# Performance work log

Measured on AMD Instinct MI355X. Metric: run time of the kernel, lower is better.

Reference implementation:

```python
import jax, jax.numpy as jnp
import numpy as np

WS = 7   # window_size
SS = 3   # shift_size = window_size // 2
NH = 16  # num_heads


def _rel_pos_index(ws):
    coords = np.stack(np.meshgrid(np.arange(ws), np.arange(ws), indexing='ij'))  # (2, ws, ws)
    cf = coords.reshape(2, -1)
    rel = (cf[:, :, None] - cf[:, None, :]).transpose(1, 2, 0)
    rel[:, :, 0] += ws - 1
    rel[:, :, 1] += ws - 1
    rel[:, :, 0] *= 2 * ws - 1
    return rel.sum(-1)  # (ws*ws, ws*ws) int

REL_IDX = _rel_pos_index(WS)


def _attn_mask(h, w, ws, ss):
    img = np.zeros((h, w))
    sls = (slice(0, -ws), slice(-ws, -ss), slice(-ss, None))
    cnt = 0
    for i in sls:
        for j in sls:
            img[i, j] = cnt
            cnt += 1
    mw = img.reshape(h // ws, ws, w // ws, ws).transpose(0, 2, 1, 3).reshape(-1, ws * ws)
    d = mw[:, None, :] - mw[:, :, None]  # (nW, N, N)
    return np.where(d != 0, -100.0, 0.0).astype(np.float32)


def _part(x, ws):
    b, h, w, c = x.shape
    return x.reshape(b, h // ws, ws, w // ws, ws, c).transpose(0, 1, 3, 2, 4, 5).reshape(-1, ws * ws, c)


def _rev(win, ws, h, w):
    c = win.shape[-1]
    b = win.shape[0] // ((h // ws) * (w // ws))
    return win.reshape(b, h // ws, w // ws, ws, ws, c).transpose(0, 1, 3, 2, 4, 5).reshape(b, h, w, c)


def _ln(x, g, b):
    m = x.mean(-1, keepdims=True)
    v = x.var(-1, keepdims=True)
    return (x - m) / jnp.sqrt(v + 1e-5) * g + b


def _wattn(x, qkv_w, qkv_b, proj_w, proj_b, table, mask):
    B_, N, C = x.shape
    hd = C // NH
    scale = hd ** -0.5
    qkv = (x @ qkv_w.T + qkv_b).reshape(B_, N, 3, NH, hd).transpose(2, 0, 3, 1, 4)
    q, k, v = qkv[0] * scale, qkv[1], qkv[2]  # (B_, NH, N, hd)
    attn = jnp.einsum('bhnd,bhmd->bhnm', q, k)
    bias = table[REL_IDX.reshape(-1)].reshape(N, N, NH).transpose(2, 0, 1)  # (NH, N, N)
    attn = attn + bias[None]
    if mask is not None:
        nW = mask.shape[0]
        attn = (attn.reshape(B_ // nW, nW, NH, N, N) + mask[None, :, None]).reshape(B_, NH, N, N)
    attn = jax.nn.softmax(attn, axis=-1)
    out = jnp.einsum('bhnm,bhmd->bhnd', attn, v).transpose(0, 2, 1, 3).reshape(B_, N, C)
    return out @ proj_w.T + proj_b


def _mlp(x, w1, b1, w2, b2):
    return jax.nn.gelu(x @ w1.T + b1, approximate=False) @ w2.T + b2


def _forward(x, w_norm1_g, w_norm1_b, w_qkv_w, w_qkv_b, w_proj_w, w_proj_b, w_table,
             w_norm2_g, w_norm2_b, w_fc1_w, w_fc1_b, w_fc2_w, w_fc2_b,
             sw_norm1_g, sw_norm1_b, sw_qkv_w, sw_qkv_b, sw_proj_w, sw_proj_b, sw_table,
             sw_norm2_g, sw_norm2_b, sw_fc1_w, sw_fc1_b, sw_fc2_w, sw_fc2_b):
    b, c, h, w = x.shape
    x = jnp.transpose(x, (0, 2, 3, 1)).reshape(b, h * w, c)  # (B, HW, C)
    shortcut = x
    xn = _ln(x, w_norm1_g, w_norm1_b).reshape(b, h, w, c)
    aw = _wattn(_part(xn, WS), w_qkv_w, w_qkv_b, w_proj_w, w_proj_b, w_table, None)
    x = shortcut + _rev(aw, WS, h, w).reshape(b, h * w, c)
    x = x + _mlp(_ln(x, w_norm2_g, w_norm2_b), w_fc1_w, w_fc1_b, w_fc2_w, w_fc2_b)
    # shifted-window branch (shift_size > 0 since min(h,w) > window_size)
    xn = _ln(x, sw_norm1_g, sw_norm1_b)
    mask = jnp.asarray(_attn_mask(h, w, WS, SS))
    shifted = jnp.roll(xn.reshape(b, h, w, c), (-SS, -SS), axis=(1, 2))
    sa = _wattn(_part(shifted, WS), sw_qkv_w, sw_qkv_b, sw_proj_w, sw_proj_b, sw_table, mask)
    shifted = jnp.roll(_rev(sa, WS, h, w), (SS, SS), axis=(1, 2)).reshape(b, h * w, c)
    # NOTE: source adds the residual to the *normalized* activations here; kept faithful.
    x = xn + shifted
    x = x + _mlp(_ln(x, sw_norm2_g, sw_norm2_b), sw_fc1_w, sw_fc1_b, sw_fc2_w, sw_fc2_b)
    return x.reshape(b, h, w, c)


def setup_inputs() -> dict:
    key = jax.random.key(0)
    ks = jax.random.split(key, 32)
    B, C, H, W = 8, 512, 56, 56
    Cm = 4 * C
    T = (2 * WS - 1) ** 2

    def rn(k, shape, s=0.02):
        return jax.random.normal(k, shape, jnp.float32) * s

    d = {'x': jax.random.normal(ks[0], (B, C, H, W), jnp.float32)}
    for i, p in enumerate(['w', 'sw']):
        o = 1 + i * 6
        d[p + '_norm1_g'] = jnp.ones((C,), jnp.float32)
        d[p + '_norm1_b'] = jnp.zeros((C,), jnp.float32)
        d[p + '_qkv_w'] = rn(ks[o], (3 * C, C))
        d[p + '_qkv_b'] = jnp.zeros((3 * C,), jnp.float32)
        d[p + '_proj_w'] = rn(ks[o + 1], (C, C))
        d[p + '_proj_b'] = jnp.zeros((C,), jnp.float32)
        d[p + '_table'] = rn(ks[o + 2], (T, NH))
        d[p + '_norm2_g'] = jnp.ones((C,), jnp.float32)
        d[p + '_norm2_b'] = jnp.zeros((C,), jnp.float32)
        d[p + '_fc1_w'] = rn(ks[o + 3], (Cm, C))
        d[p + '_fc1_b'] = jnp.zeros((Cm,), jnp.float32)
        d[p + '_fc2_w'] = rn(ks[o + 4], (C, Cm))
        d[p + '_fc2_b'] = jnp.zeros((C,), jnp.float32)
    return d


def reference(x, w_norm1_g, w_norm1_b, w_qkv_w, w_qkv_b, w_proj_w, w_proj_b, w_table,
              w_norm2_g, w_norm2_b, w_fc1_w, w_fc1_b, w_fc2_w, w_fc2_b,
              sw_norm1_g, sw_norm1_b, sw_qkv_w, sw_qkv_b, sw_proj_w, sw_proj_b, sw_table,
              sw_norm2_g, sw_norm2_b, sw_fc1_w, sw_fc1_b, sw_fc2_w, sw_fc2_b):
    return _forward(x, w_norm1_g, w_norm1_b, w_qkv_w, w_qkv_b, w_proj_w, w_proj_b, w_table,
                    w_norm2_g, w_norm2_b, w_fc1_w, w_fc1_b, w_fc2_w, w_fc2_b,
                    sw_norm1_g, sw_norm1_b, sw_qkv_w, sw_qkv_b, sw_proj_w, sw_proj_b, sw_table,
                    sw_norm2_g, sw_norm2_b, sw_fc1_w, sw_fc1_b, sw_fc2_w, sw_fc2_b)
```

## Files before the change

### kernel.cpp

```cpp
#include <hip/hip_runtime.h>
#include <hip/hip_bf16.h>

using bf16 = __hip_bfloat16;

#define B_      8
#define C_      512
#define H_      56
#define W_      56
#define HW_     3136
#define M_      25088
#define NH_     16
#define HD_     32
#define WS_     7
#define NT_     49

typedef __attribute__((ext_vector_type(8))) short bf16x8;
typedef __attribute__((ext_vector_type(4))) float f32x4;

#define AS1(p) ((const __attribute__((address_space(1))) void*)(p))
#define AS3(p) ((__attribute__((address_space(3))) void*)(p))

__device__ inline float bf2f(const bf16 v) {
    unsigned short u = *reinterpret_cast<const unsigned short*>(&v);
    return __uint_as_float((unsigned)u << 16);
}
__device__ inline unsigned short f2bfu(float f) {
    bf16 h = __float2bfloat16(f);
    return *reinterpret_cast<unsigned short*>(&h);
}
__device__ inline float rdv(const float* p) { return *p; }
__device__ inline float rdv(const bf16* p)  { return bf2f(*p); }
__device__ inline void stv(float* p, float v) { *p = v; }
__device__ inline void stv(bf16* p, float v)  { *p = __float2bfloat16(v); }

__device__ inline float gelu_t(float v) {
    const float u = v * (0.79788456080286536f + 0.035677408136300125f * v * v);
    const float e = __expf(2.0f * u);
    return 0.5f * v * (2.0f - 2.0f / (e + 1.0f));
}

__global__ void k_detect(const void* g1, int* flag) {
    const unsigned short* u = (const unsigned short*)g1;
    *flag = (u[0] == 0x3F80u) ? 1 : 0;
}

struct WArgs {
    const void* src[26];
    bf16*       dst[26];
    int         n[26];
};
__global__ __launch_bounds__(256) void k_convert_all(WArgs a, const int* flag) {
    const int isb = *flag;
    const int gid = blockIdx.x * 256 + threadIdx.x;
    const int stride = gridDim.x * 256;
    #pragma unroll 1
    for (int w = 0; w < 26; ++w) {
        const int n = a.n[w];
        bf16* d = a.dst[w];
        if (isb) {
            const unsigned short* s = (const unsigned short*)a.src[w];
            for (int i = gid; i < n; i += stride) ((unsigned short*)d)[i] = s[i];
        } else {
            const float* s = (const float*)a.src[w];
            for (int i = gid; i < n; i += stride) d[i] = __float2bfloat16(s[i]);
        }
    }
}

__global__ __launch_bounds__(256) void k_transpose_in(const void* xin, bf16* X,
                                                      const int* flag) {
    __shared__ float tile[32][33];
    const int isb = *flag;
    const int p0 = blockIdx.x * 32, c0 = blockIdx.y * 32, b = blockIdx.z;
    const int tp = threadIdx.x & 31, tc = threadIdx.x >> 5;
    const size_t ibase = (size_t)b * C_ * HW_;
    #pragma unroll
    for (int i = 0; i < 4; ++i) {
        const int c = tc + i * 8;
        const size_t idx = ibase + (size_t)(c0 + c) * HW_ + p0 + tp;
        tile[c][tp] = isb ? bf2f(((const bf16*)xin)[idx]) : ((const float*)xin)[idx];
    }
    __syncthreads();
    const int wc = threadIdx.x & 31, wp = threadIdx.x >> 5;
    bf16* dst = X + (size_t)b * HW_ * C_;
    #pragma unroll
    for (int i = 0; i < 4; ++i) {
        const int p = wp + i * 8;
        dst[(size_t)(p0 + p) * C_ + c0 + wc] = __float2bfloat16(tile[wc][p]);
    }
}

__global__ __launch_bounds__(128) void k_layernorm(const bf16* __restrict__ X,
                                                   const bf16* __restrict__ g,
                                                   const bf16* __restrict__ bta,
                                                   bf16* __restrict__ XN) {
    const int tok = blockIdx.x;
    const ushort4 u = reinterpret_cast<const ushort4*>(X + (size_t)tok * C_)[threadIdx.x];
    float4 v;
    v.x = __uint_as_float((unsigned)u.x << 16);
    v.y = __uint_as_float((unsigned)u.y << 16);
    v.z = __uint_as_float((unsigned)u.z << 16);
    v.w = __uint_as_float((unsigned)u.w << 16);
    float s  = v.x + v.y + v.z + v.w;
    float s2 = v.x * v.x + v.y * v.y + v.z * v.z + v.w * v.w;
    #pragma unroll
    for (int o = 32; o > 0; o >>= 1) { s += __shfl_down(s, o); s2 += __shfl_down(s2, o); }
    __shared__ float sh[4];
    if ((threadIdx.x & 63) == 0) { sh[threadIdx.x >> 6] = s; sh[2 + (threadIdx.x >> 6)] = s2; }
    __syncthreads();
    const float ts = sh[0] + sh[1], ts2 = sh[2] + sh[3];
    const float m = ts * (1.0f / C_);
    const float var = ts2 * (1.0f / C_) - m * m;
    const float r = rsqrtf(var + 1e-5f);
    const int c = threadIdx.x * 4;
    ushort4 o;
    o.x = f2bfu((v.x - m) * r * bf2f(g[c + 0]) + bf2f(bta[c + 0]));
    o.y = f2bfu((v.y - m) * r * bf2f(g[c + 1]) + bf2f(bta[c + 1]));
    o.z = f2bfu((v.z - m) * r * bf2f(g[c + 2]) + bf2f(bta[c + 2]));
    o.w = f2bfu((v.w - m) * r * bf2f(g[c + 3]) + bf2f(bta[c + 3]));
    reinterpret_cast<ushort4*>(XN + (size_t)tok * C_)[threadIdx.x] = o;
}

template <typename TADD, typename TO, bool GELU, bool ADD, bool FINAL>
__global__ __launch_bounds__(512, 2) void k_gemm_mfma(const bf16* __restrict__ A,
                                                      const bf16* __restrict__ Wt,
                                                      const bf16* __restrict__ bias,
                                                      const TADD* __restrict__ addp,
                                                      TO* __restrict__ out,
                                                      const int* flag,
                                                      int N, int K) {
    __shared__ bf16 sA[2][256 * 64];
    __shared__ bf16 sB[2][256 * 64];
    const int tid  = threadIdx.x;
    const int lane = tid & 63;
    const int wid  = tid >> 6;
    const int wr   = wid >> 2;
    const int wc2  = wid & 3;

    const int nwg  = gridDim.x;
    const int orig = blockIdx.x;
    const int nx = nwg >> 3, rr_ = nwg & 7;
    const int xcd = orig & 7, offw = orig >> 3;
    const int wg = (xcd < rr_ ? xcd * (nx + 1) : rr_ * (nx + 1) + (xcd - rr_) * nx) + offw;
    const int gx = N >> 8;
    const int m0 = (wg / gx) * 256, n0 = (wg % gx) * 256;

    const f32x4 vz = {0.f, 0.f, 0.f, 0.f};
    f32x4 acc[8][4];
    #pragma unroll
    for (int i = 0; i < 8; ++i)
        #pragma unroll
        for (int j = 0; j < 4; ++j) acc[i][j] = vz;

    const int sr8  = lane >> 3;
    const int schk = (lane & 7) ^ sr8;
    const bf16* gA0 = A  + (size_t)(m0 + sr8) * K + schk * 8;
    const bf16* gB0 = Wt + (size_t)(n0 + sr8) * K + schk * 8;

    const int l15 = lane & 15, g4 = lane >> 4;
    const int NTLE = K >> 6;

    int cur = 0;
    {
        #pragma unroll
        for (int p = 0; p < 4; ++p) {
            const int q = wid * 4 + p;
            __builtin_amdgcn_global_load_lds(AS1(gA0 + (size_t)(q * 8) * K),
                                             AS3(&sA[0][q * 512]), 16, 0, 0);
            __builtin_amdgcn_global_load_lds(AS1(gB0 + (size_t)(q * 8) * K),
                                             AS3(&sB[0][q * 512]), 16, 0, 0);
        }
    }

    for (int t = 0; t < NTLE; ++t) {
        asm volatile("s_waitcnt vmcnt(0)" ::: "memory");
        __builtin_amdgcn_s_barrier();

        if (t + 1 < NTLE) {
            const int kt = (t + 1) << 6;
            #pragma unroll
            for (int p = 0; p < 4; ++p) {
                const int q = wid * 4 + p;
                __builtin_amdgcn_global_load_lds(AS1(gA0 + (size_t)(q * 8) * K + kt),
                                                 AS3(&sA[cur ^ 1][q * 512]), 16, 0, 0);
                __builtin_amdgcn_global_load_lds(AS1(gB0 + (size_t)(q * 8) * K + kt),
                                                 AS3(&sB[cur ^ 1][q * 512]), 16, 0, 0);
            }
        }

        bf16x8 bfr[4][2];
        #pragma unroll
        for (int ks = 0; ks < 2; ++ks) {
            const int ch = ((ks << 2) | g4) ^ (l15 & 7);
            #pragma unroll
            for (int j = 0; j < 4; ++j) {
                const int rowB = wc2 * 64 + j * 16 + l15;
                bfr[j][ks] = *reinterpret_cast<const bf16x8*>(&sB[cur][rowB * 64 + ch * 8]);
            }
        }
        const int ch0 = g4 ^ (l15 & 7);
        const int ch1 = (4 | g4) ^ (l15 & 7);
        __builtin_amdgcn_s_setprio(1);
        #pragma unroll
        for (int i = 0; i < 8; ++i) {
            const int rowA = wr * 128 + i * 16 + l15;
            const bf16x8 a0 = *reinterpret_cast<const bf16x8*>(&sA[cur][rowA * 64 + ch0 * 8]);
            const bf16x8 a1 = *reinterpret_cast<const bf16x8*>(&sA[cur][rowA * 64 + ch1 * 8]);
            #pragma unroll
            for (int j = 0; j < 4; ++j) {
                acc[i][j] = __builtin_amdgcn_mfma_f32_16x16x32_bf16(a0, bfr[j][0], acc[i][j], 0, 0, 0);
                acc[i][j] = __builtin_amdgcn_mfma_f32_16x16x32_bf16(a1, bfr[j][1], acc[i][j], 0, 0, 0);
            }
        }
        __builtin_amdgcn_s_setprio(0);

        asm volatile("s_waitcnt lgkmcnt(0)" ::: "memory");
        __builtin_amdgcn_s_barrier();
        cur ^= 1;
    }

    int obf = 0;
    if constexpr (FINAL) obf = *flag;
    const int colBase = n0 + wc2 * 64 + l15;
    const int rowTop  = m0 + wr * 128 + g4 * 4;
    #pragma unroll
    for (int j = 0; j < 4; ++j) {
        const int col = colBase + j * 16;
        const float bc = bf2f(bias[col]);
        #pragma unroll
        for (int i = 0; i < 8; ++i) {
            #pragma unroll
            for (int r = 0; r < 4; ++r) {
                const int row = rowTop + i * 16 + r;
                float v = acc[i][j][r] + bc;
                if constexpr (GELU) v = gelu_t(v);
                if constexpr (ADD)  v += rdv(&addp[(size_t)row * N + col]);
                if constexpr (FINAL) {
                    if (obf) ((bf16*)(void*)out)[(size_t)row * N + col] = __float2bfloat16(v);
                    else     ((float*)(void*)out)[(size_t)row * N + col] = v;
                } else {
                    stv(&out[(size_t)row * N + col], v);
                }
            }
        }
    }
}

__global__ __launch_bounds__(256) void k_mktbl(const bf16* __restrict__ table,
                                               bf16* __restrict__ out, int shifted) {
    const int bh = blockIdx.x;
    const int cls = bh >> 4, h = bh & 15;
    const int rowE = shifted ? (cls >> 1) : 0;
    const int colE = shifted ? (cls & 1) : 0;
    for (int e = threadIdx.x; e < 64 * 64; e += 256) {
        const int i = e >> 6, j = e & 63;
        float v;
        if (i < NT_ && j < NT_) {
            const int yi = i / WS_, xi = i % WS_, yj = j / WS_, xj = j % WS_;
            const int ridx = (yi - yj + 6) * 13 + (xi - xj + 6);
            v = bf2f(table[ridx * NH_ + h]);
            const int ri = (rowE ? (yi < 4 ? 1 : 2) : 0) * 3 + (colE ? (xi < 4 ? 1 : 2) : 0);
            const int rj = (rowE ? (yj < 4 ? 1 : 2) : 0) * 3 + (colE ? (xj < 4 ? 1 : 2) : 0);
            if (ri != rj) v -= 100.f;
        } else if (j >= NT_) {
            v = -3e30f;
        } else {
            v = 0.f;
        }
        out[((size_t)bh << 12) + e] = __float2bfloat16(v);
    }
}

template <int SS, bool SHIFTED>
__global__ __launch_bounds__(64) void k_attn_mfma(const bf16* __restrict__ QKV,
                                                  const bf16* __restrict__ tbl,
                                                  bf16* __restrict__ O) {
    __shared__ __align__(16) short uQK[5120];
    __shared__ __align__(16) short uVt[2304];
    __shared__ int toks[NT_];
    short* Qs = uQK;
    short* Ks = uQK + 2560;
    short* Ps = uQK;

    const int lane = threadIdx.x;
    const int head = blockIdx.x & 15;
    const int win  = blockIdx.x >> 4;
    const int bl = win >> 6, w64 = win & 63;
    const int wy = w64 >> 3, wx = w64 & 7;

    if (lane < NT_) {
        const int dy = lane / WS_, dx = lane % WS_;
        const int sr = wy * WS_ + dy, scn = wx * WS_ + dx;
        const int r = (sr + SS) % H_, c = (scn + SS) % W_;
        toks[lane] = bl * HW_ + r * W_ + c;
    }
    __syncthreads();

    const int g4 = lane >> 4, l15 = lane & 15;
    const int tsg = lane >> 2, csg = (lane & 3) * 8;

    #pragma unroll
    for (int rr = 0; rr < 4; ++rr) {
        const int t = rr * 16 + tsg;
        bf16x8 qv = {0,0,0,0,0,0,0,0}, kv = {0,0,0,0,0,0,0,0}, vv = {0,0,0,0,0,0,0,0};
        if (t < NT_) {
            const bf16* base = QKV + (size_t)toks[t] * 1536 + head * HD_ + csg;
            qv = *reinterpret_cast<const bf16x8*>(base);
            kv = *reinterpret_cast<const bf16x8*>(base + 512);
            vv = *reinterpret_cast<const bf16x8*>(base + 1024);
        }
        *reinterpret_cast<bf16x8*>(&Qs[t * 40 + csg]) = qv;
        *reinterpret_cast<bf16x8*>(&Ks[t * 40 + csg]) = kv;
        #pragma unroll
        for (int e = 0; e < 8; ++e) uVt[(csg + e) * 72 + t] = ((const short*)&vv)[e];
    }
    __syncthreads();

    bf16x8 aq[4], bk[4];
    #pragma unroll
    for (int f = 0; f < 4; ++f) {
        aq[f] = *reinterpret_cast<const bf16x8*>(&Qs[(f * 16 + l15) * 40 + g4 * 8]);
        bk[f] = *reinterpret_cast<const bf16x8*>(&Ks[(f * 16 + l15) * 40 + g4 * 8]);
    }
    const f32x4 vz = {0.f, 0.f, 0.f, 0.f};
    f32x4 sacc[4][4];
    #pragma unroll
    for (int qi = 0; qi < 4; ++qi)
        #pragma unroll
        for (int kj = 0; kj < 4; ++kj)
            sacc[qi][kj] = __builtin_amdgcn_mfma_f32_16x16x32_bf16(aq[qi], bk[kj], vz, 0, 0, 0);
    __syncthreads();

    const int cls = SHIFTED ? (((wy == 7) ? 2 : 0) + ((wx == 7) ? 1 : 0)) : 0;
    const bf16* tb = tbl + (((size_t)(cls * NH_ + head)) << 12);
    const float scale = 0.17677669529663687f;
    #pragma unroll
    for (int qi = 0; qi < 4; ++qi) {
        #pragma unroll
        for (int r = 0; r < 4; ++r) {
            const int i = qi * 16 + g4 * 4 + r;
            const bf16* trow = tb + (i << 6);
            float sv[4];
            #pragma unroll
            for (int kj = 0; kj < 4; ++kj)
                sv[kj] = sacc[qi][kj][r] * scale + bf2f(trow[kj * 16 + l15]);
            float mx = fmaxf(fmaxf(sv[0], sv[1]), fmaxf(sv[2], sv[3]));
            #pragma unroll
            for (int d = 1; d <= 8; d <<= 1) mx = fmaxf(mx, __shfl_xor(mx, d));
            float p[4], sum = 0.f;
            #pragma unroll
            for (int kj = 0; kj < 4; ++kj) { p[kj] = __expf(sv[kj] - mx); sum += p[kj]; }
            #pragma unroll
            for (int d = 1; d <= 8; d <<= 1) sum += __shfl_xor(sum, d);
            const float inv = 1.0f / sum;
            #pragma unroll
            for (int kj = 0; kj < 4; ++kj)
                Ps[i * 72 + kj * 16 + l15] = (short)f2bfu(p[kj] * inv);
        }
    }
    __syncthreads();

    f32x4 oacc[4][2];
    #pragma unroll
    for (int qi = 0; qi < 4; ++qi) { oacc[qi][0] = vz; oacc[qi][1] = vz; }
    #pragma unroll
    for (int ks = 0; ks < 2; ++ks) {
        bf16x8 bv[2];
        #pragma unroll
        for (int dj = 0; dj < 2; ++dj)
            bv[dj] = *reinterpret_cast<const bf16x8*>(&uVt[(dj * 16 + l15) * 72 + ks * 32 + g4 * 8]);
        #pragma unroll
        for (int qi = 0; qi < 4; ++qi) {
            const bf16x8 ap = *reinterpret_cast<const bf16x8*>(&Ps[(qi * 16 + l15) * 72 + ks * 32 + g4 * 8]);
            #pragma unroll
            for (int dj = 0; dj < 2; ++dj)
                oacc[qi][dj] = __builtin_amdgcn_mfma_f32_16x16x32_bf16(ap, bv[dj], oacc[qi][dj], 0, 0, 0);
        }
    }
    #pragma unroll
    for (int qi = 0; qi < 4; ++qi) {
        #pragma unroll
        for (int r = 0; r < 4; ++r) {
            const int i = qi * 16 + g4 * 4 + r;
            if (i < NT_) {
                const size_t ob = (size_t)toks[i] * C_ + head * HD_ + l15;
                O[ob]      = __float2bfloat16(oacc[qi][0][r]);
                O[ob + 16] = __float2bfloat16(oacc[qi][1][r]);
            }
        }
    }
}

extern "C" void kernel_launch(void* const* d_in, const int* in_sizes, int n_in,
                              void* d_out, int out_size, void* d_ws, size_t ws_size,
                              hipStream_t stream) {
    (void)out_size; (void)ws_size;
    char* ws = (char*)d_ws;
    const size_t WEIGHT_RESERVE = 12651520;
    bf16*  WC   = (bf16*)ws;
    int*   FLG  = (int*)(ws + WEIGHT_RESERVE);
    bf16*  TBL1 = (bf16*)(ws + WEIGHT_RESERVE + 1024);
    bf16*  TBL2 = (bf16*)(ws + WEIGHT_RESERVE + 1024 + 131072);
    bf16*  X    = (bf16*)(ws + WEIGHT_RESERVE + 656384);
    bf16*  XN   = X + (size_t)M_ * C_;
    char*  BIG  = (char*)(XN + (size_t)M_ * C_);

    size_t offs[27];
    size_t off = 0;
    for (int i = 1; i < n_in && i < 27; ++i) { offs[i] = off; off += (size_t)((in_sizes[i] + 7) & ~7); }
    auto wc = [&](int i) { return (const bf16*)(WC + offs[i]); };

    k_detect<<<1, 1, 0, stream>>>(d_in[1], FLG);
    {
        WArgs a;
        for (int i = 1; i < 27; ++i) {
            a.src[i - 1] = d_in[i];
            a.dst[i - 1] = WC + offs[i];
            a.n[i - 1]   = in_sizes[i];
        }
        k_convert_all<<<512, 256, 0, stream>>>(a, FLG);
    }
    k_mktbl<<<16, 256, 0, stream>>>(wc(7),  TBL1, 0);
    k_mktbl<<<64, 256, 0, stream>>>(wc(20), TBL2, 1);

    const dim3 gT(HW_ / 32, C_ / 32, B_);
    k_transpose_in<<<gT, 256, 0, stream>>>(d_in[0], X, FLG);

    bf16* QKV = (bf16*)BIG;
    bf16* ATT = (bf16*)(BIG + (size_t)M_ * 1536 * 2);
    bf16* HID = (bf16*)BIG;

    const int gQ = (1536 / 256) * (M_ / 256);
    const int gP = (512 / 256)  * (M_ / 256);
    const int gF = (2048 / 256) * (M_ / 256);
    const dim3 gA(B_ * 64 * NH_);

    k_layernorm<<<M_, 128, 0, stream>>>(X, wc(1), wc(2), XN);
    k_gemm_mfma<bf16, bf16, false, false, false><<<gQ, 512, 0, stream>>>(
        XN, wc(3), wc(4), (const bf16*)nullptr, QKV, nullptr, 1536, C_);
    k_attn_mfma<0, false><<<gA, 64, 0, stream>>>(QKV, TBL1, ATT);
    k_gemm_mfma<bf16, bf16, false, true, false><<<gP, 512, 0, stream>>>(
        ATT, wc(5), wc(6), X, X, nullptr, C_, C_);
    k_layernorm<<<M_, 128, 0, stream>>>(X, wc(8), wc(9), XN);
    k_gemm_mfma<bf16, bf16, true, false, false><<<gF, 512, 0, stream>>>(
        XN, wc(10), wc(11), (const bf16*)nullptr, HID, nullptr, 2048, C_);
    k_gemm_mfma<bf16, bf16, false, true, false><<<gP, 512, 0, stream>>>(
        HID, wc(12), wc(13), X, X, nullptr, C_, 2048);
    k_layernorm<<<M_, 128, 0, stream>>>(X, wc(14), wc(15), XN);
    k_gemm_mfma<bf16, bf16, false, false, false><<<gQ, 512, 0, stream>>>(
        XN, wc(16), wc(17), (const bf16*)nullptr, QKV, nullptr, 1536, C_);
    k_attn_mfma<3, true><<<gA, 64, 0, stream>>>(QKV, TBL2, ATT);
    k_gemm_mfma<bf16, bf16, false, true, false><<<gP, 512, 0, stream>>>(
        ATT, wc(18), wc(19), XN, X, nullptr, C_, C_);
    k_layernorm<<<M_, 128, 0, stream>>>(X, wc(21), wc(22), XN);
    k_gemm_mfma<bf16, bf16, true, false, false><<<gF, 512, 0, stream>>>(
        XN, wc(23), wc(24), (const bf16*)nullptr, HID, nullptr, 2048, C_);
    k_gemm_mfma<bf16, float, false, true, true><<<gP, 512, 0, stream>>>(
        HID, wc(25), wc(26), X, (float*)d_out, FLG, C_, 2048);
}
```

Before: 910.5 us.

## Split GEMM into shallow-K high-occupancy and 128x128 tile variants

Replaces the single 256x256x64 GEMM kernel with two variants. The first keeps 256x256 output tiles but uses a 32-deep K slice, halving LDS use so four workgroups can fit per CU. The second uses 128x128 tiles with 256 threads for the N=512 projection and fc2 GEMMs, giving more workgroups to fill the GPU where the 256-wide tiling produced few blocks. It also reorders the epilogue so the bias values are loaded once up front. The cost is more barrier iterations per K in the first variant and less operand reuse per tile in the second.

```diff
diff --git a/kernel.cpp b/kernel.cpp
--- a/kernel.cpp
+++ b/kernel.cpp
@@ -122,15 +122,15 @@
 }
 
 template <typename TADD, typename TO, bool GELU, bool ADD, bool FINAL>
-__global__ __launch_bounds__(512, 2) void k_gemm_mfma(const bf16* __restrict__ A,
-                                                      const bf16* __restrict__ Wt,
-                                                      const bf16* __restrict__ bias,
-                                                      const TADD* __restrict__ addp,
-                                                      TO* __restrict__ out,
-                                                      const int* flag,
-                                                      int N, int K) {
-    __shared__ bf16 sA[2][256 * 64];
-    __shared__ bf16 sB[2][256 * 64];
+__global__ __launch_bounds__(512, 4) void k_gemm_mfma_a(const bf16* __restrict__ A,
+                                                        const bf16* __restrict__ Wt,
+                                                        const bf16* __restrict__ bias,
+                                                        const TADD* __restrict__ addp,
+                                                        TO* __restrict__ out,
+                                                        const int* flag,
+                                                        int N, int K) {
+    __shared__ bf16 sA[2][256 * 32];
+    __shared__ bf16 sB[2][256 * 32];
     const int tid  = threadIdx.x;
     const int lane = tid & 63;
     const int wid  = tid >> 6;
@@ -152,6 +152,125 @@
         #pragma unroll
         for (int j = 0; j < 4; ++j) acc[i][j] = vz;
 
+    const int sr16 = lane >> 2;
+    const int schk = (lane & 3) ^ ((lane >> 3) & 3);
+    const bf16* gA0 = A  + (size_t)(m0 + sr16) * K + schk * 8;
+    const bf16* gB0 = Wt + (size_t)(n0 + sr16) * K + schk * 8;
+
+    const int l15 = lane & 15, g4 = lane >> 4;
+    const int NT32 = K >> 5;
+
+    int cur = 0;
+    {
+        #pragma unroll
+        for (int p = 0; p < 2; ++p) {
+            const int q = wid * 2 + p;
+            __builtin_amdgcn_global_load_lds(AS1(gA0 + (size_t)(q * 16) * K),
+                                             AS3(&sA[0][q * 512]), 16, 0, 0);
+            __builtin_amdgcn_global_load_lds(AS1(gB0 + (size_t)(q * 16) * K),
+                                             AS3(&sB[0][q * 512]), 16, 0, 0);
+        }
+    }
+
+    for (int t = 0; t < NT32; ++t) {
+        asm volatile("s_waitcnt vmcnt(0)" ::: "memory");
+        __builtin_amdgcn_s_barrier();
+
+        if (t + 1 < NT32) {
+            const int kt = (t + 1) << 5;
+            #pragma unroll
+            for (int p = 0; p < 2; ++p) {
+                const int q = wid * 2 + p;
+                __builtin_amdgcn_global_load_lds(AS1(gA0 + (size_t)(q * 16) * K + kt),
+                                                 AS3(&sA[cur ^ 1][q * 512]), 16, 0, 0);
+                __builtin_amdgcn_global_load_lds(AS1(gB0 + (size_t)(q * 16) * K + kt),
+                                                 AS3(&sB[cur ^ 1][q * 512]), 16, 0, 0);
+            }
+        }
+
+        const int ch = g4 ^ ((l15 >> 1) & 3);
+        bf16x8 bfr[4];
+        #pragma unroll
+        for (int j = 0; j < 4; ++j) {
+            const int rowB = wc2 * 64 + j * 16 + l15;
+            bfr[j] = *reinterpret_cast<const bf16x8*>(&sB[cur][rowB * 32 + ch * 8]);
+        }
+        __builtin_amdgcn_s_setprio(1);
+        #pragma unroll
+        for (int i = 0; i < 8; ++i) {
+            const int rowA = wr * 128 + i * 16 + l15;
+            const bf16x8 a0 = *reinterpret_cast<const bf16x8*>(&sA[cur][rowA * 32 + ch * 8]);
+            #pragma unroll
+            for (int j = 0; j < 4; ++j)
+                acc[i][j] = __builtin_amdgcn_mfma_f32_16x16x32_bf16(a0, bfr[j], acc[i][j], 0, 0, 0);
+        }
+        __builtin_amdgcn_s_setprio(0);
+
+        asm volatile("s_waitcnt lgkmcnt(0)" ::: "memory");
+        __builtin_amdgcn_s_barrier();
+        cur ^= 1;
+    }
+
+    int obf = 0;
+    if constexpr (FINAL) obf = *flag;
+    const int colBase = n0 + wc2 * 64 + l15;
+    const int rowTop  = m0 + wr * 128 + g4 * 4;
+    float bc[4];
+    #pragma unroll
+    for (int j = 0; j < 4; ++j) bc[j] = bf2f(bias[colBase + j * 16]);
+    #pragma unroll
+    for (int i = 0; i < 8; ++i) {
+        #pragma unroll
+        for (int r = 0; r < 4; ++r) {
+            const int row = rowTop + i * 16 + r;
+            #pragma unroll
+            for (int j = 0; j < 4; ++j) {
+                const int col = colBase + j * 16;
+                float v = acc[i][j][r] + bc[j];
+                if constexpr (GELU) v = gelu_t(v);
+                if constexpr (ADD)  v += rdv(&addp[(size_t)row * N + col]);
+                if constexpr (FINAL) {
+                    if (obf) ((bf16*)(void*)out)[(size_t)row * N + col] = __float2bfloat16(v);
+                    else     ((float*)(void*)out)[(size_t)row * N + col] = v;
+                } else {
+                    stv(&out[(size_t)row * N + col], v);
+                }
+            }
+        }
+    }
+}
+
+template <typename TADD, typename TO, bool GELU, bool ADD, bool FINAL>
+__global__ __launch_bounds__(256, 2) void k_gemm_mfma_b(const bf16* __restrict__ A,
+                                                        const bf16* __restrict__ Wt,
+                                                        const bf16* __restrict__ bias,
+                                                        const TADD* __restrict__ addp,
+                                                        TO* __restrict__ out,
+                                                        const int* flag,
+                                                        int N, int K) {
+    __shared__ bf16 sA[2][128 * 64];
+    __shared__ bf16 sB[2][128 * 64];
+    const int tid  = threadIdx.x;
+    const int lane = tid & 63;
+    const int wid  = tid >> 6;
+    const int wr   = wid >> 1;
+    const int wc2  = wid & 1;
+
+    const int nwg  = gridDim.x;
+    const int orig = blockIdx.x;
+    const int nx = nwg >> 3, rr_ = nwg & 7;
+    const int xcd = orig & 7, offw = orig >> 3;
+    const int wg = (xcd < rr_ ? xcd * (nx + 1) : rr_ * (nx + 1) + (xcd - rr_) * nx) + offw;
+    const int gx = N >> 7;
+    const int m0 = (wg / gx) * 128, n0 = (wg % gx) * 128;
+
+    const f32x4 vz = {0.f, 0.f, 0.f, 0.f};
+    f32x4 acc[4][4];
+    #pragma unroll
+    for (int i = 0; i < 4; ++i)
+        #pragma unroll
+        for (int j = 0; j < 4; ++j) acc[i][j] = vz;
+
     const int sr8  = lane >> 3;
     const int schk = (lane & 7) ^ sr8;
     const bf16* gA0 = A  + (size_t)(m0 + sr8) * K + schk * 8;
@@ -188,30 +307,27 @@
             }
         }
 
-        bf16x8 bfr[4][2];
+        bf16x8 af[4][2], bf_[4][2];
         #pragma unroll
         for (int ks = 0; ks < 2; ++ks) {
             const int ch = ((ks << 2) | g4) ^ (l15 & 7);
             #pragma unroll
+            for (int f = 0; f < 4; ++f) {
+                const int rowA = wr * 64 + f * 16 + l15;
+                af[f][ks] = *reinterpret_cast<const bf16x8*>(&sA[cur][rowA * 64 + ch * 8]);
+                const int rowB = wc2 * 64 + f * 16 + l15;
+                bf_[f][ks] = *reinterpret_cast<const bf16x8*>(&sB[cur][rowB * 64 + ch * 8]);
+            }
+        }
+
+        __builtin_amdgcn_s_setprio(1);
+        #pragma unroll
+        for (int i = 0; i < 4; ++i)
+            #pragma unroll
             for (int j = 0; j < 4; ++j) {
-                const int rowB = wc2 * 64 + j * 16 + l15;
-                bfr[j][ks] = *reinterpret_cast<const bf16x8*>(&sB[cur][rowB * 64 + ch * 8]);
-            }
-        }
-        const int ch0 = g4 ^ (l15 & 7);
-        const int ch1 = (4 | g4) ^ (l15 & 7);
-        __builtin_amdgcn_s_setprio(1);
-        #pragma unroll
-        for (int i = 0; i < 8; ++i) {
-            const int rowA = wr * 128 + i * 16 + l15;
-            const bf16x8 a0 = *reinterpret_cast<const bf16x8*>(&sA[cur][rowA * 64 + ch0 * 8]);
-            const bf16x8 a1 = *reinterpret_cast<const bf16x8*>(&sA[cur][rowA * 64 + ch1 * 8]);
-            #pragma unroll
-            for (int j = 0; j < 4; ++j) {
-                acc[i][j] = __builtin_amdgcn_mfma_f32_16x16x32_bf16(a0, bfr[j][0], acc[i][j], 0, 0, 0);
-                acc[i][j] = __builtin_amdgcn_mfma_f32_16x16x32_bf16(a1, bfr[j][1], acc[i][j], 0, 0, 0);
-            }
-        }
+                acc[i][j] = __builtin_amdgcn_mfma_f32_16x16x32_bf16(af[i][0], bf_[j][0], acc[i][j], 0, 0, 0);
+                acc[i][j] = __builtin_amdgcn_mfma_f32_16x16x32_bf16(af[i][1], bf_[j][1], acc[i][j], 0, 0, 0);
+            }
         __builtin_amdgcn_s_setprio(0);
 
         asm volatile("s_waitcnt lgkmcnt(0)" ::: "memory");
@@ -222,17 +338,19 @@
     int obf = 0;
     if constexpr (FINAL) obf = *flag;
     const int colBase = n0 + wc2 * 64 + l15;
-    const int rowTop  = m0 + wr * 128 + g4 * 4;
-    #pragma unroll
-    for (int j = 0; j < 4; ++j) {
-        const int col = colBase + j * 16;
-        const float bc = bf2f(bias[col]);
-        #pragma unroll
-        for (int i = 0; i < 8; ++i) {
-            #pragma unroll
-            for (int r = 0; r < 4; ++r) {
-                const int row = rowTop + i * 16 + r;
-                float v = acc[i][j][r] + bc;
+    const int rowTop  = m0 + wr * 64 + g4 * 4;
+    float bc[4];
+    #pragma unroll
+    for (int j = 0; j < 4; ++j) bc[j] = bf2f(bias[colBase + j * 16]);
+    #pragma unroll
+    for (int i = 0; i < 4; ++i) {
+        #pragma unroll
+        for (int r = 0; r < 4; ++r) {
+            const int row = rowTop + i * 16 + r;
+            #pragma unroll
+            for (int j = 0; j < 4; ++j) {
+                const int col = colBase + j * 16;
+                float v = acc[i][j][r] + bc[j];
                 if constexpr (GELU) v = gelu_t(v);
                 if constexpr (ADD)  v += rdv(&addp[(size_t)row * N + col]);
                 if constexpr (FINAL) {
@@ -431,30 +549,30 @@
     bf16* HID = (bf16*)BIG;
 
     const int gQ = (1536 / 256) * (M_ / 256);
-    const int gP = (512 / 256)  * (M_ / 256);
     const int gF = (2048 / 256) * (M_ / 256);
+    const int gP = (512 / 128)  * (M_ / 128);
     const dim3 gA(B_ * 64 * NH_);
 
     k_layernorm<<<M_, 128, 0, stream>>>(X, wc(1), wc(2), XN);
-    k_gemm_mfma<bf16, bf16, false, false, false><<<gQ, 512, 0, stream>>>(
+    k_gemm_mfma_a<bf16, bf16, false, false, false><<<gQ, 512, 0, stream>>>(
         XN, wc(3), wc(4), (const bf16*)nullptr, QKV, nullptr, 1536, C_);
     k_attn_mfma<0, false><<<gA, 64, 0, stream>>>(QKV, TBL1, ATT);
-    k_gemm_mfma<bf16, bf16, false, true, false><<<gP, 512, 0, stream>>>(
+    k_gemm_mfma_b<bf16, bf16, false, true, false><<<gP, 256, 0, stream>>>(
         ATT, wc(5), wc(6), X, X, nullptr, C_, C_);
     k_layernorm<<<M_, 128, 0, stream>>>(X, wc(8), wc(9), XN);
-    k_gemm_mfma<bf16, bf16, true, false, false><<<gF, 512, 0, stream>>>(
+    k_gemm_mfma_a<bf16, bf16, true, false, false><<<gF, 512, 0, stream>>>(
         XN, wc(10), wc(11), (const bf16*)nullptr, HID, nullptr, 2048, C_);
-    k_gemm_mfma<bf16, bf16, false, true, false><<<gP, 512, 0, stream>>>(
+    k_gemm_mfma_b<bf16, bf16, false, true, false><<<gP, 256, 0, stream>>>(
         HID, wc(12), wc(13), X, X, nullptr, C_, 2048);
     k_layernorm<<<M_, 128, 0, stream>>>(X, wc(14), wc(15), XN);
-    k_gemm_mfma<bf16, bf16, false, false, false><<<gQ, 512, 0, stream>>>(
+    k_gemm_mfma_a<bf16, bf16, false, false, false><<<gQ, 512, 0, stream>>>(
         XN, wc(16), wc(17), (const bf16*)nullptr, QKV, nullptr, 1536, C_);
     k_attn_mfma<3, true><<<gA, 64, 0, stream>>>(QKV, TBL2, ATT);
-    k_gemm_mfma<bf16, bf16, false, true, false><<<gP, 512, 0, stream>>>(
+    k_gemm_mfma_b<bf16, bf16, false, true, false><<<gP, 256, 0, stream>>>(
         ATT, wc(18), wc(19), XN, X, nullptr, C_, C_);
     k_layernorm<<<M_, 128, 0, stream>>>(X, wc(21), wc(22), XN);
-    k_gemm_mfma<bf16, bf16, true, false, false><<<gF, 512, 0, stream>>>(
+    k_gemm_mfma_a<bf16, bf16, true, false, false><<<gF, 512, 0, stream>>>(
         XN, wc(23), wc(24), (const bf16*)nullptr, HID, nullptr, 2048, C_);
-    k_gemm_mfma<bf16, float, false, true, true><<<gP, 512, 0, stream>>>(
+    k_gemm_mfma_b<bf16, float, false, true, true><<<gP, 256, 0, stream>>>(
         HID, wc(25), wc(26), X, (float*)d_out, FLG, C_, 2048);
 }
```

Measured after the change: 1.912 ms. 2.1x slower.

## Use 256x128 GEMM tiles with triple-buffered LDS prefetch and partial vmcnt waits

Applied to the files above, without the earlier changes.

Shrinks the GEMM tile from 256x256 to 256x128, halving per-wave accumulators and doubling the grid. Replaces the double buffer with a three-stage LDS ring, issuing loads three tiles ahead and waiting with partial vmcnt counts so global loads overlap compute. Also reorders the epilogue loops and hoists the bias loads. LDS use per block rises to about 144KB, which may limit occupancy, and the smaller tile lowers arithmetic intensity.

```diff
diff --git a/kernel.cpp b/kernel.cpp
--- a/kernel.cpp
+++ b/kernel.cpp
@@ -129,26 +129,26 @@
                                                       TO* __restrict__ out,
                                                       const int* flag,
                                                       int N, int K) {
-    __shared__ bf16 sA[2][256 * 64];
-    __shared__ bf16 sB[2][256 * 64];
+    __shared__ bf16 sA[3][256 * 64];
+    __shared__ bf16 sB[3][128 * 64];
     const int tid  = threadIdx.x;
     const int lane = tid & 63;
     const int wid  = tid >> 6;
-    const int wr   = wid >> 2;
-    const int wc2  = wid & 3;
+    const int wr   = wid >> 1;
+    const int wc2  = wid & 1;
 
     const int nwg  = gridDim.x;
     const int orig = blockIdx.x;
     const int nx = nwg >> 3, rr_ = nwg & 7;
     const int xcd = orig & 7, offw = orig >> 3;
     const int wg = (xcd < rr_ ? xcd * (nx + 1) : rr_ * (nx + 1) + (xcd - rr_) * nx) + offw;
-    const int gx = N >> 8;
-    const int m0 = (wg / gx) * 256, n0 = (wg % gx) * 256;
+    const int gx = N >> 7;
+    const int m0 = (wg / gx) * 256, n0 = (wg % gx) * 128;
 
     const f32x4 vz = {0.f, 0.f, 0.f, 0.f};
-    f32x4 acc[8][4];
-    #pragma unroll
-    for (int i = 0; i < 8; ++i)
+    f32x4 acc[4][4];
+    #pragma unroll
+    for (int i = 0; i < 4; ++i)
         #pragma unroll
         for (int j = 0; j < 4; ++j) acc[i][j] = vz;
 
@@ -160,79 +160,94 @@
     const int l15 = lane & 15, g4 = lane >> 4;
     const int NTLE = K >> 6;
 
-    int cur = 0;
-    {
+    #pragma unroll
+    for (int tt = 0; tt < 3; ++tt) {
+        const int kt = tt << 6;
         #pragma unroll
         for (int p = 0; p < 4; ++p) {
             const int q = wid * 4 + p;
-            __builtin_amdgcn_global_load_lds(AS1(gA0 + (size_t)(q * 8) * K),
-                                             AS3(&sA[0][q * 512]), 16, 0, 0);
-            __builtin_amdgcn_global_load_lds(AS1(gB0 + (size_t)(q * 8) * K),
-                                             AS3(&sB[0][q * 512]), 16, 0, 0);
+            __builtin_amdgcn_global_load_lds(AS1(gA0 + (size_t)(q * 8) * K + kt),
+                                             AS3(&sA[tt][q * 512]), 16, 0, 0);
+        }
+        #pragma unroll
+        for (int p = 0; p < 2; ++p) {
+            const int q = wid * 2 + p;
+            __builtin_amdgcn_global_load_lds(AS1(gB0 + (size_t)(q * 8) * K + kt),
+                                             AS3(&sB[tt][q * 512]), 16, 0, 0);
         }
     }
 
     for (int t = 0; t < NTLE; ++t) {
-        asm volatile("s_waitcnt vmcnt(0)" ::: "memory");
+        const int rem = NTLE - 1 - t;
+        if (rem >= 2)      asm volatile("s_waitcnt vmcnt(12)" ::: "memory");
+        else if (rem == 1) asm volatile("s_waitcnt vmcnt(6)"  ::: "memory");
+        else               asm volatile("s_waitcnt vmcnt(0)"  ::: "memory");
         __builtin_amdgcn_s_barrier();
 
-        if (t + 1 < NTLE) {
-            const int kt = (t + 1) << 6;
+        const int buf = t % 3;
+        bf16x8 bfr[4][2];
+        #pragma unroll
+        for (int ks = 0; ks < 2; ++ks) {
+            const int ch = ((ks << 2) | g4) ^ (l15 & 7);
+            #pragma unroll
+            for (int j = 0; j < 4; ++j) {
+                const int rowB = wc2 * 64 + j * 16 + l15;
+                bfr[j][ks] = *reinterpret_cast<const bf16x8*>(&sB[buf][rowB * 64 + ch * 8]);
+            }
+        }
+        const int ch0 = g4 ^ (l15 & 7);
+        const int ch1 = (4 | g4) ^ (l15 & 7);
+        __builtin_amdgcn_s_setprio(1);
+        #pragma unroll
+        for (int i = 0; i < 4; ++i) {
+            const int rowA = wr * 64 + i * 16 + l15;
+            const bf16x8 a0 = *reinterpret_cast<const bf16x8*>(&sA[buf][rowA * 64 + ch0 * 8]);
+            const bf16x8 a1 = *reinterpret_cast<const bf16x8*>(&sA[buf][rowA * 64 + ch1 * 8]);
+            #pragma unroll
+            for (int j = 0; j < 4; ++j) {
+                acc[i][j] = __builtin_amdgcn_mfma_f32_16x16x32_bf16(a0, bfr[j][0], acc[i][j], 0, 0, 0);
+                acc[i][j] = __builtin_amdgcn_mfma_f32_16x16x32_bf16(a1, bfr[j][1], acc[i][j], 0, 0, 0);
+            }
+        }
+        __builtin_amdgcn_s_setprio(0);
+
+        asm volatile("s_waitcnt lgkmcnt(0)" ::: "memory");
+        __builtin_amdgcn_s_barrier();
+
+        const int tn = t + 3;
+        if (tn < NTLE) {
+            const int kt = tn << 6;
             #pragma unroll
             for (int p = 0; p < 4; ++p) {
                 const int q = wid * 4 + p;
                 __builtin_amdgcn_global_load_lds(AS1(gA0 + (size_t)(q * 8) * K + kt),
-                                                 AS3(&sA[cur ^ 1][q * 512]), 16, 0, 0);
+                                                 AS3(&sA[buf][q * 512]), 16, 0, 0);
+            }
+            #pragma unroll
+            for (int p = 0; p < 2; ++p) {
+                const int q = wid * 2 + p;
                 __builtin_amdgcn_global_load_lds(AS1(gB0 + (size_t)(q * 8) * K + kt),
-                                                 AS3(&sB[cur ^ 1][q * 512]), 16, 0, 0);
-            }
-        }
-
-        bf16x8 bfr[4][2];
-        #pragma unroll
-        for (int ks = 0; ks < 2; ++ks) {
-            const int ch = ((ks << 2) | g4) ^ (l15 & 7);
-            #pragma unroll
-            for (int j = 0; j < 4; ++j) {
-                const int rowB = wc2 * 64 + j * 16 + l15;
-                bfr[j][ks] = *reinterpret_cast<const bf16x8*>(&sB[cur][rowB * 64 + ch * 8]);
-            }
-        }
-        const int ch0 = g4 ^ (l15 & 7);
-        const int ch1 = (4 | g4) ^ (l15 & 7);
-        __builtin_amdgcn_s_setprio(1);
-        #pragma unroll
-        for (int i = 0; i < 8; ++i) {
-            const int rowA = wr * 128 + i * 16 + l15;
-            const bf16x8 a0 = *reinterpret_cast<const bf16x8*>(&sA[cur][rowA * 64 + ch0 * 8]);
-            const bf16x8 a1 = *reinterpret_cast<const bf16x8*>(&sA[cur][rowA * 64 + ch1 * 8]);
-            #pragma unroll
-            for (int j = 0; j < 4; ++j) {
-                acc[i][j] = __builtin_amdgcn_mfma_f32_16x16x32_bf16(a0, bfr[j][0], acc[i][j], 0, 0, 0);
-                acc[i][j] = __builtin_amdgcn_mfma_f32_16x16x32_bf16(a1, bfr[j][1], acc[i][j], 0, 0, 0);
-            }
-        }
-        __builtin_amdgcn_s_setprio(0);
-
-        asm volatile("s_waitcnt lgkmcnt(0)" ::: "memory");
-        __builtin_amdgcn_s_barrier();
-        cur ^= 1;
+                                                 AS3(&sB[buf][q * 512]), 16, 0, 0);
+            }
+        }
     }
 
     int obf = 0;
     if constexpr (FINAL) obf = *flag;
     const int colBase = n0 + wc2 * 64 + l15;
-    const int rowTop  = m0 + wr * 128 + g4 * 4;
-    #pragma unroll
-    for (int j = 0; j < 4; ++j) {
-        const int col = colBase + j * 16;
-        const float bc = bf2f(bias[col]);
-        #pragma unroll
-        for (int i = 0; i < 8; ++i) {
-            #pragma unroll
-            for (int r = 0; r < 4; ++r) {
-                const int row = rowTop + i * 16 + r;
-                float v = acc[i][j][r] + bc;
+    const int rowTop  = m0 + wr * 64 + g4 * 4;
+    float bc[4];
+    #pragma unroll
+    for (int j = 0; j < 4; ++j) bc[j] = bf2f(bias[colBase + j * 16]);
+    #pragma unroll
+    for (int i = 0; i < 4; ++i) {
+        #pragma unroll
+        for (int r = 0; r < 4; ++r) {
+            const int row = rowTop + i * 16 + r;
+            #pragma unroll
+            for (int j = 0; j < 4; ++j) {
+                const int col = colBase + j * 16;
+                float v = acc[i][j][r] + bc[j];
                 if constexpr (GELU) v = gelu_t(v);
                 if constexpr (ADD)  v += rdv(&addp[(size_t)row * N + col]);
                 if constexpr (FINAL) {
@@ -430,9 +445,9 @@
     bf16* ATT = (bf16*)(BIG + (size_t)M_ * 1536 * 2);
     bf16* HID = (bf16*)BIG;
 
-    const int gQ = (1536 / 256) * (M_ / 256);
-    const int gP = (512 / 256)  * (M_ / 256);
-    const int gF = (2048 / 256) * (M_ / 256);
+    const int gQ = (1536 / 128) * (M_ / 256);
+    const int gP = (512 / 128)  * (M_ / 256);
+    const int gF = (2048 / 128) * (M_ / 256);
     const dim3 gA(B_ * 64 * NH_);
 
     k_layernorm<<<M_, 128, 0, stream>>>(X, wc(1), wc(2), XN);
```

New measurement: 849.3 us. 6.7% less time.
